# Optimization experiments

Hardware: AMD Instinct MI355X
Metric: run time of the kernel (lower is better)

Reference implementation:

```python
import jax, jax.numpy as jnp
import numpy as np

N = 100000   # nodes
E = 1600000  # edges
D = 128      # feature dim (layers all 128)
G = 512      # graphs in batch
C = 10       # num_classes
EPS = 1e-5   # batchnorm eps


def setup_inputs() -> dict:
    key = jax.random.key(0)
    ks = jax.random.split(key, 16)
    s = 1.0 / np.sqrt(D)
    return {
        "x": jax.random.normal(ks[0], (N, D), jnp.float32),
        "edge_index": jax.random.randint(ks[1], (2, E), 0, N),
        "batch": jnp.sort(jax.random.randint(ks[2], (N,), 0, G)),
        "w1": jax.random.normal(ks[3], (D, D), jnp.float32) * s,
        "b1": jnp.zeros((D,), jnp.float32),
        "w2": jax.random.normal(ks[4], (D, D), jnp.float32) * s,
        "b2": jnp.zeros((D,), jnp.float32),
        "w3": jax.random.normal(ks[5], (D, D), jnp.float32) * s,
        "b3": jnp.zeros((D,), jnp.float32),
        "g1": jnp.ones((D,), jnp.float32),
        "be1": jnp.zeros((D,), jnp.float32),
        "g2": jnp.ones((D,), jnp.float32),
        "be2": jnp.zeros((D,), jnp.float32),
        "fc_w": jax.random.normal(ks[6], (D, C), jnp.float32) * s,
        "fc_b": jnp.zeros((C,), jnp.float32),
    }


def _gcn(x, src, dst, norm, W, b):
    # transform -> gather -> normalize -> scatter-add (PyG GCNConv)
    h = x @ W
    out = jax.ops.segment_sum(h[src] * norm[:, None], dst, num_segments=x.shape[0])
    return out + b


def _bn(x, g, b):
    # training-mode BatchNorm1d: batch mean / biased variance
    mu = jnp.mean(x, axis=0)
    var = jnp.mean((x - mu) ** 2, axis=0)
    return (x - mu) * jax.lax.rsqrt(var + EPS) * g + b


def reference(x, edge_index, batch, w1, b1, w2, b2, w3, b3, g1, be1, g2, be2, fc_w, fc_b):
    n = x.shape[0]
    loop = jnp.arange(n)
    src = jnp.concatenate([edge_index[0], loop])  # add self-loops
    dst = jnp.concatenate([edge_index[1], loop])
    deg = jax.ops.segment_sum(jnp.ones_like(src, x.dtype), dst, num_segments=n)
    dinv = jax.lax.rsqrt(jnp.maximum(deg, 1.0))  # deg >= 1 due to self-loops
    norm = dinv[src] * dinv[dst]  # symmetric normalization per edge

    h = jax.nn.relu(_gcn(x, src, dst, norm, w1, b1))        # conv1 + relu (bn1 unused, per source)
    h = jax.nn.relu(_gcn(h, src, dst, norm, w2, b2))        # conv2 + relu
    h = jax.nn.relu(_bn(h, g1, be1))                        # bn + relu
    h = jax.nn.relu(_gcn(h, src, dst, norm, w3, b3))        # conv3 + relu
    h = jax.nn.relu(_bn(h, g2, be2))                        # bn + relu

    cnt = jax.ops.segment_sum(jnp.ones((n,), h.dtype), batch, num_segments=G)
    pooled = jax.ops.segment_sum(h, batch, num_segments=G) / jnp.maximum(cnt, 1.0)[:, None]
    logits = pooled @ fc_w + fc_b
    return jax.nn.log_softmax(logits, axis=1)
```

## Files before the change

kernel.cpp:

```cpp
#include <hip/hip_runtime.h>
#include <hip/hip_bf16.h>
#include <math.h>

#define D 128
#define G_GRAPHS 512
#define C_CLASSES 10
#define BN_EPS 1e-5f
#define NBUCK_MAX 512
#define EDGE_CHUNK 4096
#define EPT 16

typedef unsigned short u16;
typedef unsigned int u32;
typedef unsigned short ushort4_t __attribute__((ext_vector_type(4)));
typedef unsigned short ushort8_t __attribute__((ext_vector_type(8)));
typedef __bf16 bf16x8 __attribute__((ext_vector_type(8)));
typedef float floatx4 __attribute__((ext_vector_type(4)));
union B8 { ushort8_t u; bf16x8 b; };

__device__ __forceinline__ float bf_lo(u32 v) { return __uint_as_float(v << 16); }
__device__ __forceinline__ float bf_hi(u32 v) { return __uint_as_float(v & 0xffff0000u); }
__device__ __forceinline__ u16 f2bf(float f) {
    union { float f; u32 u; } x; x.f = f;
    u32 r = x.u + 0x7fff + ((x.u >> 16) & 1);
    return (u16)(r >> 16);
}
__device__ __forceinline__ u32 pack2bf(float a, float b) {
    return (u32)f2bf(a) | ((u32)f2bf(b) << 16);
}


__global__ __launch_bounds__(256) void bucket_hist_kernel(
    const int* __restrict__ dst, int* __restrict__ bucketCnt, int E, int nbuck)
{
    __shared__ int h[NBUCK_MAX];
    int tid = threadIdx.x;
    for (int i = tid; i < NBUCK_MAX; i += 256) h[i] = 0;
    __syncthreads();
    for (int i = blockIdx.x * 256 + tid; i < E; i += gridDim.x * 256)
        atomicAdd(&h[dst[i] >> 8], 1);
    __syncthreads();
    for (int i = tid; i < nbuck; i += 256)
        if (h[i]) atomicAdd(&bucketCnt[i], h[i]);
}

__global__ void scan_buckets_kernel(
    const int* __restrict__ bucketCnt, int* __restrict__ bucketBase,
    int* __restrict__ bucketCursor, int* __restrict__ rowPtr, int nbuck, int N, int E)
{
    __shared__ int buf[2][512];
    int tid = threadIdx.x;
    int v = (tid < nbuck) ? bucketCnt[tid] : 0;
    buf[0][tid] = v;
    __syncthreads();
    int cur = 0;
    for (int off = 1; off < 512; off <<= 1) {
        buf[1 - cur][tid] = buf[cur][tid] + ((tid >= off) ? buf[cur][tid - off] : 0);
        cur ^= 1;
        __syncthreads();
    }
    if (tid < nbuck) {
        int b = buf[cur][tid] - v;
        bucketBase[tid] = b;
        bucketCursor[tid] = b;
    }
    if (tid == 0) { bucketBase[nbuck] = E; rowPtr[N] = E; }
}

__global__ __launch_bounds__(256) void scatter_pairs_kernel(
    const int* __restrict__ src, const int* __restrict__ dst,
    int* __restrict__ bucketCursor, u32* __restrict__ pairs, int E)
{
    __shared__ int h[NBUCK_MAX];
    __shared__ int base[NBUCK_MAX];
    int tid = threadIdx.x;
    int e0 = blockIdx.x * EDGE_CHUNK;
    for (int i = tid; i < NBUCK_MAX; i += 256) h[i] = 0;
    __syncthreads();
    int s[EPT], d[EPT], r[EPT];
#pragma unroll
    for (int j = 0; j < EPT; ++j) {
        int i = e0 + j * 256 + tid;
        if (i < E) {
            s[j] = src[i];
            d[j] = dst[i];
            r[j] = atomicAdd(&h[d[j] >> 8], 1);
        } else {
            d[j] = -1;
        }
    }
    __syncthreads();
    for (int i = tid; i < NBUCK_MAX; i += 256)
        if (h[i]) base[i] = atomicAdd(&bucketCursor[i], h[i]);
    __syncthreads();
#pragma unroll
    for (int j = 0; j < EPT; ++j) {
        if (d[j] >= 0) {
            int b = d[j] >> 8;
            pairs[base[b] + r[j]] = ((u32)s[j] << 8) | (u32)(d[j] & 255);
        }
    }
}

__global__ __launch_bounds__(256) void bucket_sort_kernel(
    const u32* __restrict__ pairs, const int* __restrict__ bucketBase,
    int* __restrict__ colIdx, int* __restrict__ rowPtr, float* __restrict__ dinv, int N)
{
    __shared__ int h[256];
    __shared__ int cur[256];
    __shared__ int sbuf[2][256];
    int tid = threadIdx.x;
    int b = blockIdx.x;
    int s = bucketBase[b], e = bucketBase[b + 1];
    h[tid] = 0;
    __syncthreads();
    for (int i = s + tid; i < e; i += 256)
        atomicAdd(&h[pairs[i] & 255], 1);
    __syncthreads();
    int cnt = h[tid];
    sbuf[0][tid] = cnt;
    __syncthreads();
    int c = 0;
    for (int off = 1; off < 256; off <<= 1) {
        sbuf[1 - c][tid] = sbuf[c][tid] + ((tid >= off) ? sbuf[c][tid - off] : 0);
        c ^= 1;
        __syncthreads();
    }
    int excl = sbuf[c][tid] - cnt;
    int v = b * 256 + tid;
    if (v < N) {
        rowPtr[v] = s + excl;
        dinv[v] = rsqrtf((float)(cnt + 1));
    }
    cur[tid] = s + excl;
    __syncthreads();
    for (int i = s + tid; i < e; i += 256) {
        u32 p = pairs[i];
        int pos = atomicAdd(&cur[p & 255], 1);
        colIdx[pos] = (int)(p >> 8);
    }
}

__global__ __launch_bounds__(256) void graph_bounds_kernel(
    const int* __restrict__ batch, int* __restrict__ gstart, int N)
{
    int i = blockIdx.x * 256 + threadIdx.x;
    if (i >= N) return;
    int b = batch[i];
    int prev = (i == 0) ? -1 : batch[i - 1];
    if (b != prev) {
        for (int g = prev + 1; g <= b; ++g) gstart[g] = i;
    }
    if (i == N - 1) {
        for (int g = b + 1; g <= G_GRAPHS; ++g) gstart[g] = N;
    }
}

__global__ __launch_bounds__(256) void wconv_kernel(
    const float4* __restrict__ w1, const float4* __restrict__ w2,
    const float4* __restrict__ w3, u16* __restrict__ wtAll)
{
    const float4* W = (blockIdx.x == 0) ? w1 : (blockIdx.x == 1) ? w2 : w3;
    u16* Wt = wtAll + (size_t)blockIdx.x * D * D;
    int tid = threadIdx.x;
#pragma unroll
    for (int i = 0; i < 16; ++i) {
        int idx = tid + i * 256;
        int k = idx >> 5, c4 = idx & 31;
        float4 v = W[idx];
        Wt[(4 * c4 + 0) * D + k] = f2bf(v.x);
        Wt[(4 * c4 + 1) * D + k] = f2bf(v.y);
        Wt[(4 * c4 + 2) * D + k] = f2bf(v.z);
        Wt[(4 * c4 + 3) * D + k] = f2bf(v.w);
    }
}

#define XS_STRIDE 136
#define GEMM_GRID 768

__device__ __forceinline__ void gemm_core_and_store(
    const u16* Xs, const u16* Ws, u16* __restrict__ Y, int row0, int nrows, int tid)
{
    int wid = tid >> 6, lane = tid & 63;
    int m = lane & 15, quad = lane >> 4;
    int xrow = wid * 16 + m;

    floatx4 acc[8] = {};
#pragma unroll
    for (int ks = 0; ks < 4; ++ks) {
        int kk = ks * 32 + quad * 8;
        B8 a;
        a.u = *(const ushort8_t*)&Xs[xrow * XS_STRIDE + kk];
#pragma unroll
        for (int t = 0; t < 8; ++t) {
            B8 b;
            b.u = *(const ushort8_t*)&Ws[(t * 16 + m) * XS_STRIDE + kk];
            acc[t] = __builtin_amdgcn_mfma_f32_16x16x32_bf16(b.b, a.b, acc[t], 0, 0, 0);
        }
    }
    int grow = row0 + xrow;
    if (grow < nrows) {
#pragma unroll
        for (int t = 0; t < 8; ++t) {
            ushort4_t o;
            o.x = f2bf(acc[t][0]); o.y = f2bf(acc[t][1]);
            o.z = f2bf(acc[t][2]); o.w = f2bf(acc[t][3]);
            *(ushort4_t*)&Y[(size_t)grow * D + t * 16 + quad * 4] = o;
        }
    }
}

__device__ __forceinline__ void stage_w(const u16* __restrict__ Wt, u16* Ws, int tid) {
    const ushort8_t* Wv = (const ushort8_t*)Wt;
#pragma unroll
    for (int i = 0; i < 8; ++i) {
        int idx = tid + i * 256;
        int n = idx >> 4, c8 = idx & 15;
        *(ushort8_t*)&Ws[n * XS_STRIDE + c8 * 8] = Wv[idx];
    }
}

__global__ __launch_bounds__(256) void gemm_mfma_f32in_kernel(
    const float4* __restrict__ X, const u16* __restrict__ Wt,
    u16* __restrict__ Y, int nrows, int ntiles)
{
    __shared__ __align__(16) u16 Xs[64 * XS_STRIDE];
    __shared__ __align__(16) u16 Ws[128 * XS_STRIDE];
    int tid = threadIdx.x;
    stage_w(Wt, Ws, tid);
    for (int t = blockIdx.x; t < ntiles; t += gridDim.x) {
        int row0 = t * 64;
        __syncthreads();
#pragma unroll
        for (int i = 0; i < 8; ++i) {
            int idx = tid + i * 256;
            int r = idx >> 5, c4 = idx & 31;
            int gr = row0 + r;
            float4 v = make_float4(0.f, 0.f, 0.f, 0.f);
            if (gr < nrows) v = X[(size_t)gr * 32 + c4];
            ushort4_t o;
            o.x = f2bf(v.x); o.y = f2bf(v.y); o.z = f2bf(v.z); o.w = f2bf(v.w);
            *(ushort4_t*)&Xs[r * XS_STRIDE + c4 * 4] = o;
        }
        __syncthreads();
        gemm_core_and_store(Xs, Ws, Y, row0, nrows, tid);
    }
}

__global__ __launch_bounds__(256) void gemm_mfma_bf16in_kernel(
    const uint4* __restrict__ X, const u16* __restrict__ Wt,
    const float* __restrict__ gsum, const float* __restrict__ gsq,
    const float* __restrict__ gamma, const float* __restrict__ beta, float invN,
    u16* __restrict__ Y, int nrows, int ntiles)
{
    __shared__ __align__(16) u16 Xs[64 * XS_STRIDE];
    __shared__ __align__(16) u16 Ws[128 * XS_STRIDE];
    __shared__ float scs[D], shs[D];
    int tid = threadIdx.x;
    bool fuse = (gsum != nullptr);
    stage_w(Wt, Ws, tid);
    if (fuse && tid < D) {
        float mu = gsum[tid] * invN;
        float var = gsq[tid] * invN - mu * mu;
        float sc = gamma[tid] * rsqrtf(var + BN_EPS);
        scs[tid] = sc;
        shs[tid] = beta[tid] - mu * sc;
    }
    for (int t = blockIdx.x; t < ntiles; t += gridDim.x) {
        int row0 = t * 64;
        __syncthreads();
#pragma unroll
        for (int i = 0; i < 4; ++i) {
            int idx = tid + i * 256;
            int r = idx >> 4, c8 = idx & 15;
            int gr = row0 + r;
            uint4 v = make_uint4(0, 0, 0, 0);
            if (gr < nrows) v = X[(size_t)gr * 16 + c8];
            if (fuse) {
                int k = c8 * 8;
                v.x = pack2bf(fmaxf(bf_lo(v.x) * scs[k]     + shs[k],     0.f),
                              fmaxf(bf_hi(v.x) * scs[k + 1] + shs[k + 1], 0.f));
                v.y = pack2bf(fmaxf(bf_lo(v.y) * scs[k + 2] + shs[k + 2], 0.f),
                              fmaxf(bf_hi(v.y) * scs[k + 3] + shs[k + 3], 0.f));
                v.z = pack2bf(fmaxf(bf_lo(v.z) * scs[k + 4] + shs[k + 4], 0.f),
                              fmaxf(bf_hi(v.z) * scs[k + 5] + shs[k + 5], 0.f));
                v.w = pack2bf(fmaxf(bf_lo(v.w) * scs[k + 6] + shs[k + 6], 0.f),
                              fmaxf(bf_hi(v.w) * scs[k + 7] + shs[k + 7], 0.f));
            }
            *(uint4*)&Xs[r * XS_STRIDE + c8 * 8] = v;
        }
        __syncthreads();
        gemm_core_and_store(Xs, Ws, Y, row0, nrows, tid);
    }
}

#define ACC8(tw, duu)                                              \
    acc[0] += (duu) * bf_lo((tw).x); acc[1] += (duu) * bf_hi((tw).x); \
    acc[2] += (duu) * bf_lo((tw).y); acc[3] += (duu) * bf_hi((tw).y); \
    acc[4] += (duu) * bf_lo((tw).z); acc[5] += (duu) * bf_hi((tw).z); \
    acc[6] += (duu) * bf_lo((tw).w); acc[7] += (duu) * bf_hi((tw).w);

__global__ __launch_bounds__(256) void aggregate_kernel(
    const uint4* __restrict__ T, const int* __restrict__ colIdx,
    const int* __restrict__ rowPtr, const float* __restrict__ dinv,
    const float* __restrict__ bias, u32* __restrict__ outH, int n)
{
    int wid = threadIdx.x >> 6;
    int lane = threadIdx.x & 63;
    int row = blockIdx.x * 4 + wid;
    if (row >= n) return;
    int fg = lane & 15;
    int eg = lane >> 4;
    const char* baseT = (const char*)T + fg * 16;

    float dr = dinv[row];
    float acc[8] = {};

    if (eg == 0) {
        uint4 sv = T[(size_t)row * 16 + fg];
        acc[0] = dr * bf_lo(sv.x); acc[1] = dr * bf_hi(sv.x);
        acc[2] = dr * bf_lo(sv.y); acc[3] = dr * bf_hi(sv.y);
        acc[4] = dr * bf_lo(sv.z); acc[5] = dr * bf_hi(sv.z);
        acc[6] = dr * bf_lo(sv.w); acc[7] = dr * bf_hi(sv.w);
    }

    int s = rowPtr[row], e = rowPtr[row + 1];
    for (int j0 = s; j0 < e; j0 += 64) {
        int m = e - j0;
        if (m > 64) m = 64;
        u32 voff = (u32)row << 8;
        float du = 0.f;
        if (lane < m) {
            int u = colIdx[j0 + lane];
            voff = (u32)u << 8;
            du = dinv[u];
        }
        int nc = (m + 15) >> 4;
        for (int c = 0; c < nc; ++c) {
            int b0 = c * 16 + eg;
            u32 o0 = (u32)__shfl((int)voff, b0);      u32 o1 = (u32)__shfl((int)voff, b0 + 4);
            u32 o2 = (u32)__shfl((int)voff, b0 + 8);  u32 o3 = (u32)__shfl((int)voff, b0 + 12);
            float d0 = __shfl(du, b0);      float d1 = __shfl(du, b0 + 4);
            float d2 = __shfl(du, b0 + 8);  float d3 = __shfl(du, b0 + 12);
            uint4 t0 = *(const uint4*)(baseT + o0);
            uint4 t1 = *(const uint4*)(baseT + o1);
            uint4 t2 = *(const uint4*)(baseT + o2);
            uint4 t3 = *(const uint4*)(baseT + o3);
            ACC8(t0, d0); ACC8(t1, d1); ACC8(t2, d2); ACC8(t3, d3);
        }
    }

#pragma unroll
    for (int off = 16; off < 64; off <<= 1) {
#pragma unroll
        for (int i = 0; i < 8; ++i) acc[i] += __shfl_xor(acc[i], off);
    }

    const float2* bp = (const float2*)bias;
    int pidx = fg * 4 + eg;
    float2 b = bp[pidx];
    float ox = fmaxf(dr * acc[eg * 2] + b.x, 0.f);
    float oy = fmaxf(dr * acc[eg * 2 + 1] + b.y, 0.f);
    outH[(size_t)row * 64 + pidx] = pack2bf(ox, oy);
}

__global__ __launch_bounds__(256) void bn_stats_kernel(
    const u32* __restrict__ H, int n, float* __restrict__ gsum, float* __restrict__ gsq)
{
    int tid = threadIdx.x;
    int c = tid & 63, rr = tid >> 6;
    float sA = 0.f, sA2 = 0.f, sB = 0.f, sB2 = 0.f;
    for (int row = blockIdx.x * 4 + rr; row < n; row += gridDim.x * 4) {
        u32 v = H[(size_t)row * 64 + c];
        float a = bf_lo(v), b = bf_hi(v);
        sA += a; sA2 += a * a; sB += b; sB2 += b * b;
    }
    __shared__ float shA[256], shA2[256], shB[256], shB2[256];
    shA[tid] = sA; shA2[tid] = sA2; shB[tid] = sB; shB2[tid] = sB2;
    __syncthreads();
    if (tid < 64) {
        float tA = shA[tid] + shA[tid + 64] + shA[tid + 128] + shA[tid + 192];
        float tA2 = shA2[tid] + shA2[tid + 64] + shA2[tid + 128] + shA2[tid + 192];
        float tB = shB[tid] + shB[tid + 64] + shB[tid + 128] + shB[tid + 192];
        float tB2 = shB2[tid] + shB2[tid + 64] + shB2[tid + 128] + shB2[tid + 192];
        atomicAdd(&gsum[2 * c], tA);
        atomicAdd(&gsq[2 * c], tA2);
        atomicAdd(&gsum[2 * c + 1], tB);
        atomicAdd(&gsq[2 * c + 1], tB2);
    }
}

__global__ __launch_bounds__(256) void pool_classify_kernel(
    const u32* __restrict__ H, const float* __restrict__ gsum, const float* __restrict__ gsq,
    const float* __restrict__ gamma, const float* __restrict__ beta, float invN,
    const int* __restrict__ gstart, const float* __restrict__ fcw,
    const float* __restrict__ fcb, float* __restrict__ out)
{
    int g = blockIdx.x;
    int tid = threadIdx.x;
    int c = tid & 63, q = tid >> 6;
    float muA = gsum[2 * c] * invN, muB = gsum[2 * c + 1] * invN;
    float vA = gsq[2 * c] * invN - muA * muA, vB = gsq[2 * c + 1] * invN - muB * muB;
    float scA = gamma[2 * c] * rsqrtf(vA + BN_EPS), scB = gamma[2 * c + 1] * rsqrtf(vB + BN_EPS);
    float shA = beta[2 * c] - muA * scA, shB = beta[2 * c + 1] - muB * scB;

    int s = gstart[g], cnt = gstart[g + 1] - s;
    float aA = 0.f, aB = 0.f;
    for (int i = q; i < cnt; i += 4) {
        u32 v = H[(size_t)(s + i) * 64 + c];
        aA += fmaxf(bf_lo(v) * scA + shA, 0.f);
        aB += fmaxf(bf_hi(v) * scB + shB, 0.f);
    }
    __shared__ float sA[256], sB[256];
    __shared__ float prow[D];
    __shared__ float lg[C_CLASSES];
    sA[tid] = aA; sB[tid] = aB;
    __syncthreads();
    if (tid < 64) {
        float tA = sA[tid] + sA[tid + 64] + sA[tid + 128] + sA[tid + 192];
        float tB = sB[tid] + sB[tid + 64] + sB[tid + 128] + sB[tid + 192];
        float inv = 1.f / (float)(cnt > 1 ? cnt : 1);
        prow[2 * tid] = tA * inv;
        prow[2 * tid + 1] = tB * inv;
    }
    __syncthreads();
    if (tid < C_CLASSES) {
        float sum = fcb[tid];
        for (int d = 0; d < D; ++d) sum += prow[d] * fcw[d * C_CLASSES + tid];
        lg[tid] = sum;
    }
    __syncthreads();
    if (tid == 0) {
        float mx = -1e30f;
        for (int k = 0; k < C_CLASSES; ++k) mx = fmaxf(mx, lg[k]);
        float se = 0.f;
        for (int k = 0; k < C_CLASSES; ++k) se += expf(lg[k] - mx);
        float lse = mx + logf(se);
        for (int k = 0; k < C_CLASSES; ++k) out[(size_t)g * C_CLASSES + k] = lg[k] - lse;
    }
}

extern "C" void kernel_launch(void* const* d_in, const int* in_sizes, int n_in,
                              void* d_out, int out_size, void* d_ws, size_t ws_size,
                              hipStream_t stream) {
    const float* x   = (const float*)d_in[0];
    const int* ei    = (const int*)d_in[1];
    const int* batch = (const int*)d_in[2];
    const float* w1  = (const float*)d_in[3];
    const float* b1  = (const float*)d_in[4];
    const float* w2  = (const float*)d_in[5];
    const float* b2  = (const float*)d_in[6];
    const float* w3  = (const float*)d_in[7];
    const float* b3  = (const float*)d_in[8];
    const float* g1  = (const float*)d_in[9];
    const float* be1 = (const float*)d_in[10];
    const float* g2  = (const float*)d_in[11];
    const float* be2 = (const float*)d_in[12];
    const float* fcw = (const float*)d_in[13];
    const float* fcb = (const float*)d_in[14];

    const int N = in_sizes[0] / D;
    const int E = in_sizes[1] / 2;
    const int* src = ei;
    const int* dst = ei + E;
    const int nbuck = (N + 255) >> 8;
    const float invN = 1.f / (float)N;

    char* p = (char*)d_ws;
    auto alloc = [&](size_t bytes) -> void* {
        void* r = (void*)p;
        p += (bytes + 255) & ~(size_t)255;
        return r;
    };
    int*   bucketCnt    = (int*)alloc(NBUCK_MAX * 4);
    float* statsacc     = (float*)alloc(4 * D * 4);
    float* gsum1 = statsacc, *gsq1 = statsacc + D, *gsum2 = statsacc + 2 * D, *gsq2 = statsacc + 3 * D;
    float* dinv     = (float*)alloc((size_t)N * 4);
    int*   rowPtr   = (int*)alloc((size_t)(N + 1) * 4);
    int*   colIdx   = (int*)alloc((size_t)E * 4);
    u32*   pairs    = (u32*)alloc((size_t)E * 4);
    int*   bucketBase   = (int*)alloc((NBUCK_MAX + 1) * 4);
    int*   bucketCursor = (int*)alloc(NBUCK_MAX * 4);
    int*   gstart  = (int*)alloc((G_GRAPHS + 1) * 4);
    u16*   wtAll   = (u16*)alloc((size_t)3 * D * D * 2);
    u16*   tmp     = (u16*)alloc((size_t)N * D * 2);
    u16*   hbuf    = (u16*)alloc((size_t)N * D * 2);

    hipMemsetAsync(bucketCnt, 0, NBUCK_MAX * 4 + 4 * D * 4, stream);

    bucket_hist_kernel<<<512, 256, 0, stream>>>(dst, bucketCnt, E, nbuck);
    scan_buckets_kernel<<<1, 512, 0, stream>>>(bucketCnt, bucketBase, bucketCursor, rowPtr, nbuck, N, E);
    scatter_pairs_kernel<<<(E + EDGE_CHUNK - 1) / EDGE_CHUNK, 256, 0, stream>>>(src, dst, bucketCursor, pairs, E);
    bucket_sort_kernel<<<nbuck, 256, 0, stream>>>(pairs, bucketBase, colIdx, rowPtr, dinv, N);
    graph_bounds_kernel<<<(N + 255) / 256, 256, 0, stream>>>(batch, gstart, N);
    wconv_kernel<<<3, 256, 0, stream>>>((const float4*)w1, (const float4*)w2, (const float4*)w3, wtAll);

    const int NT = (N + 63) / 64;
    const int GB = NT < GEMM_GRID ? NT : GEMM_GRID;
    const int AB = (N + 3) / 4;

    gemm_mfma_f32in_kernel<<<GB, 256, 0, stream>>>((const float4*)x, wtAll, tmp, N, NT);
    aggregate_kernel<<<AB, 256, 0, stream>>>((const uint4*)tmp, colIdx, rowPtr, dinv, b1, (u32*)hbuf, N);
    gemm_mfma_bf16in_kernel<<<GB, 256, 0, stream>>>((const uint4*)hbuf, wtAll + D * D,
        nullptr, nullptr, nullptr, nullptr, 0.f, tmp, N, NT);
    aggregate_kernel<<<AB, 256, 0, stream>>>((const uint4*)tmp, colIdx, rowPtr, dinv, b2, (u32*)hbuf, N);
    bn_stats_kernel<<<256, 256, 0, stream>>>((const u32*)hbuf, N, gsum1, gsq1);
    gemm_mfma_bf16in_kernel<<<GB, 256, 0, stream>>>((const uint4*)hbuf, wtAll + 2 * D * D,
        gsum1, gsq1, g1, be1, invN, tmp, N, NT);
    aggregate_kernel<<<AB, 256, 0, stream>>>((const uint4*)tmp, colIdx, rowPtr, dinv, b3, (u32*)hbuf, N);
    bn_stats_kernel<<<256, 256, 0, stream>>>((const u32*)hbuf, N, gsum2, gsq2);
    pool_classify_kernel<<<G_GRAPHS, 256, 0, stream>>>((const u32*)hbuf, gsum2, gsq2, g2, be2, invN,
        gstart, fcw, fcb, (float*)d_out);
}
```

Before: 509.1 us.

## Prescale GEMM output by source dinv and use 16-lane-per-row aggregation

The GEMM epilogue now multiplies each output row by dinv of that node. The aggregation then no longer has to load dinv[u] per edge or multiply by it, and just sums the gathered rows. The aggregate kernel is also restructured so that 16 lanes handle one destination row, 16 rows per block, walking edges serially with 4-way unrolling. This removes the shuffles and the cross-lane reduction. In exchange it gives less edge-level parallelism per row and more load imbalance across high-degree rows, and the prescaled values are rounded to bf16 at a different point.

```diff
diff --git a/kernel.cpp b/kernel.cpp
--- a/kernel.cpp
+++ b/kernel.cpp
@@ -179,7 +179,8 @@
 #define GEMM_GRID 768
 
 __device__ __forceinline__ void gemm_core_and_store(
-    const u16* Xs, const u16* Ws, u16* __restrict__ Y, int row0, int nrows, int tid)
+    const u16* Xs, const u16* Ws, const float* __restrict__ dinv,
+    u16* __restrict__ Y, int row0, int nrows, int tid)
 {
     int wid = tid >> 6, lane = tid & 63;
     int m = lane & 15, quad = lane >> 4;
@@ -200,11 +201,12 @@
     }
     int grow = row0 + xrow;
     if (grow < nrows) {
+        float du = dinv[grow];
 #pragma unroll
         for (int t = 0; t < 8; ++t) {
             ushort4_t o;
-            o.x = f2bf(acc[t][0]); o.y = f2bf(acc[t][1]);
-            o.z = f2bf(acc[t][2]); o.w = f2bf(acc[t][3]);
+            o.x = f2bf(acc[t][0] * du); o.y = f2bf(acc[t][1] * du);
+            o.z = f2bf(acc[t][2] * du); o.w = f2bf(acc[t][3] * du);
             *(ushort4_t*)&Y[(size_t)grow * D + t * 16 + quad * 4] = o;
         }
     }
@@ -222,7 +224,7 @@
 
 __global__ __launch_bounds__(256) void gemm_mfma_f32in_kernel(
     const float4* __restrict__ X, const u16* __restrict__ Wt,
-    u16* __restrict__ Y, int nrows, int ntiles)
+    const float* __restrict__ dinv, u16* __restrict__ Y, int nrows, int ntiles)
 {
     __shared__ __align__(16) u16 Xs[64 * XS_STRIDE];
     __shared__ __align__(16) u16 Ws[128 * XS_STRIDE];
@@ -243,7 +245,7 @@
             *(ushort4_t*)&Xs[r * XS_STRIDE + c4 * 4] = o;
         }
         __syncthreads();
-        gemm_core_and_store(Xs, Ws, Y, row0, nrows, tid);
+        gemm_core_and_store(Xs, Ws, dinv, Y, row0, nrows, tid);
     }
 }
 
@@ -251,7 +253,7 @@
     const uint4* __restrict__ X, const u16* __restrict__ Wt,
     const float* __restrict__ gsum, const float* __restrict__ gsq,
     const float* __restrict__ gamma, const float* __restrict__ beta, float invN,
-    u16* __restrict__ Y, int nrows, int ntiles)
+    const float* __restrict__ dinv, u16* __restrict__ Y, int nrows, int ntiles)
 {
     __shared__ __align__(16) u16 Xs[64 * XS_STRIDE];
     __shared__ __align__(16) u16 Ws[128 * XS_STRIDE];
@@ -290,78 +292,66 @@
             *(uint4*)&Xs[r * XS_STRIDE + c8 * 8] = v;
         }
         __syncthreads();
-        gemm_core_and_store(Xs, Ws, Y, row0, nrows, tid);
-    }
-}
-
-#define ACC8(tw, duu)                                              \
-    acc[0] += (duu) * bf_lo((tw).x); acc[1] += (duu) * bf_hi((tw).x); \
-    acc[2] += (duu) * bf_lo((tw).y); acc[3] += (duu) * bf_hi((tw).y); \
-    acc[4] += (duu) * bf_lo((tw).z); acc[5] += (duu) * bf_hi((tw).z); \
-    acc[6] += (duu) * bf_lo((tw).w); acc[7] += (duu) * bf_hi((tw).w);
+        gemm_core_and_store(Xs, Ws, dinv, Y, row0, nrows, tid);
+    }
+}
+
+#define ACCV(tw)                                       \
+    acc0 += bf_lo((tw).x); acc1 += bf_hi((tw).x);      \
+    acc2 += bf_lo((tw).y); acc3 += bf_hi((tw).y);      \
+    acc4 += bf_lo((tw).z); acc5 += bf_hi((tw).z);      \
+    acc6 += bf_lo((tw).w); acc7 += bf_hi((tw).w);
 
 __global__ __launch_bounds__(256) void aggregate_kernel(
     const uint4* __restrict__ T, const int* __restrict__ colIdx,
     const int* __restrict__ rowPtr, const float* __restrict__ dinv,
     const float* __restrict__ bias, u32* __restrict__ outH, int n)
 {
-    int wid = threadIdx.x >> 6;
-    int lane = threadIdx.x & 63;
-    int row = blockIdx.x * 4 + wid;
+    int tid = threadIdx.x;
+    int fg = tid & 15;
+    int grp = tid >> 4;
+    int row = blockIdx.x * 16 + grp;
     if (row >= n) return;
-    int fg = lane & 15;
-    int eg = lane >> 4;
+
     const char* baseT = (const char*)T + fg * 16;
 
+    uint4 sv = *(const uint4*)(baseT + ((size_t)(u32)row << 8));
+    float acc0 = bf_lo(sv.x), acc1 = bf_hi(sv.x);
+    float acc2 = bf_lo(sv.y), acc3 = bf_hi(sv.y);
+    float acc4 = bf_lo(sv.z), acc5 = bf_hi(sv.z);
+    float acc6 = bf_lo(sv.w), acc7 = bf_hi(sv.w);
+
+    int s = rowPtr[row], e = rowPtr[row + 1];
+    int j = s;
+    for (; j + 4 <= e; j += 4) {
+        int u0 = colIdx[j];
+        int u1 = colIdx[j + 1];
+        int u2 = colIdx[j + 2];
+        int u3 = colIdx[j + 3];
+        uint4 t0 = *(const uint4*)(baseT + ((size_t)(u32)u0 << 8));
+        uint4 t1 = *(const uint4*)(baseT + ((size_t)(u32)u1 << 8));
+        uint4 t2 = *(const uint4*)(baseT + ((size_t)(u32)u2 << 8));
+        uint4 t3 = *(const uint4*)(baseT + ((size_t)(u32)u3 << 8));
+        ACCV(t0); ACCV(t1); ACCV(t2); ACCV(t3);
+    }
+    for (; j < e; ++j) {
+        int u = colIdx[j];
+        uint4 t = *(const uint4*)(baseT + ((size_t)(u32)u << 8));
+        ACCV(t);
+    }
+
     float dr = dinv[row];
-    float acc[8] = {};
-
-    if (eg == 0) {
-        uint4 sv = T[(size_t)row * 16 + fg];
-        acc[0] = dr * bf_lo(sv.x); acc[1] = dr * bf_hi(sv.x);
-        acc[2] = dr * bf_lo(sv.y); acc[3] = dr * bf_hi(sv.y);
-        acc[4] = dr * bf_lo(sv.z); acc[5] = dr * bf_hi(sv.z);
-        acc[6] = dr * bf_lo(sv.w); acc[7] = dr * bf_hi(sv.w);
-    }
-
-    int s = rowPtr[row], e = rowPtr[row + 1];
-    for (int j0 = s; j0 < e; j0 += 64) {
-        int m = e - j0;
-        if (m > 64) m = 64;
-        u32 voff = (u32)row << 8;
-        float du = 0.f;
-        if (lane < m) {
-            int u = colIdx[j0 + lane];
-            voff = (u32)u << 8;
-            du = dinv[u];
-        }
-        int nc = (m + 15) >> 4;
-        for (int c = 0; c < nc; ++c) {
-            int b0 = c * 16 + eg;
-            u32 o0 = (u32)__shfl((int)voff, b0);      u32 o1 = (u32)__shfl((int)voff, b0 + 4);
-            u32 o2 = (u32)__shfl((int)voff, b0 + 8);  u32 o3 = (u32)__shfl((int)voff, b0 + 12);
-            float d0 = __shfl(du, b0);      float d1 = __shfl(du, b0 + 4);
-            float d2 = __shfl(du, b0 + 8);  float d3 = __shfl(du, b0 + 12);
-            uint4 t0 = *(const uint4*)(baseT + o0);
-            uint4 t1 = *(const uint4*)(baseT + o1);
-            uint4 t2 = *(const uint4*)(baseT + o2);
-            uint4 t3 = *(const uint4*)(baseT + o3);
-            ACC8(t0, d0); ACC8(t1, d1); ACC8(t2, d2); ACC8(t3, d3);
-        }
-    }
-
-#pragma unroll
-    for (int off = 16; off < 64; off <<= 1) {
-#pragma unroll
-        for (int i = 0; i < 8; ++i) acc[i] += __shfl_xor(acc[i], off);
-    }
-
     const float2* bp = (const float2*)bias;
-    int pidx = fg * 4 + eg;
-    float2 b = bp[pidx];
-    float ox = fmaxf(dr * acc[eg * 2] + b.x, 0.f);
-    float oy = fmaxf(dr * acc[eg * 2 + 1] + b.y, 0.f);
-    outH[(size_t)row * 64 + pidx] = pack2bf(ox, oy);
+    float2 b0 = bp[fg * 4 + 0];
+    float2 b1 = bp[fg * 4 + 1];
+    float2 b2 = bp[fg * 4 + 2];
+    float2 b3 = bp[fg * 4 + 3];
+    uint4 o;
+    o.x = pack2bf(fmaxf(dr * acc0 + b0.x, 0.f), fmaxf(dr * acc1 + b0.y, 0.f));
+    o.y = pack2bf(fmaxf(dr * acc2 + b1.x, 0.f), fmaxf(dr * acc3 + b1.y, 0.f));
+    o.z = pack2bf(fmaxf(dr * acc4 + b2.x, 0.f), fmaxf(dr * acc5 + b2.y, 0.f));
+    o.w = pack2bf(fmaxf(dr * acc6 + b3.x, 0.f), fmaxf(dr * acc7 + b3.y, 0.f));
+    *(uint4*)&outH[(size_t)row * 64 + fg * 4] = o;
 }
 
 __global__ __launch_bounds__(256) void bn_stats_kernel(
@@ -497,16 +487,16 @@
 
     const int NT = (N + 63) / 64;
     const int GB = NT < GEMM_GRID ? NT : GEMM_GRID;
-    const int AB = (N + 3) / 4;
-
-    gemm_mfma_f32in_kernel<<<GB, 256, 0, stream>>>((const float4*)x, wtAll, tmp, N, NT);
+    const int AB = (N + 15) / 16;
+
+    gemm_mfma_f32in_kernel<<<GB, 256, 0, stream>>>((const float4*)x, wtAll, dinv, tmp, N, NT);
     aggregate_kernel<<<AB, 256, 0, stream>>>((const uint4*)tmp, colIdx, rowPtr, dinv, b1, (u32*)hbuf, N);
     gemm_mfma_bf16in_kernel<<<GB, 256, 0, stream>>>((const uint4*)hbuf, wtAll + D * D,
-        nullptr, nullptr, nullptr, nullptr, 0.f, tmp, N, NT);
+        nullptr, nullptr, nullptr, nullptr, 0.f, dinv, tmp, N, NT);
     aggregate_kernel<<<AB, 256, 0, stream>>>((const uint4*)tmp, colIdx, rowPtr, dinv, b2, (u32*)hbuf, N);
     bn_stats_kernel<<<256, 256, 0, stream>>>((const u32*)hbuf, N, gsum1, gsq1);
     gemm_mfma_bf16in_kernel<<<GB, 256, 0, stream>>>((const uint4*)hbuf, wtAll + 2 * D * D,
-        gsum1, gsq1, g1, be1, invN, tmp, N, NT);
+        gsum1, gsq1, g1, be1, invN, dinv, tmp, N, NT);
     aggregate_kernel<<<AB, 256, 0, stream>>>((const uint4*)tmp, colIdx, rowPtr, dinv, b3, (u32*)hbuf, N);
     bn_stats_kernel<<<256, 256, 0, stream>>>((const u32*)hbuf, N, gsum2, gsq2);
     pool_classify_kernel<<<G_GRAPHS, 256, 0, stream>>>((const u32*)hbuf, gsum2, gsq2, g2, be2, invN,
```

After: 507.8 us. Within noise of the previous version (-0.3%).
